# Kernel tuning notes

Measured on AMD Instinct MI355X. Metric: run time of the kernel, lower is better.

The kernel has to match this reference:

```python
import jax, jax.numpy as jnp
import numpy as np
import math

B, N, H, OUT = 32, 2048, 256, 128
K = 6            # knn_graph k
ALPHA = 0.2      # GCN2Conv alpha (beta=1 since theta/layer are None)
NEG = 0.2        # leaky_relu negative slope in ASAP
EPS = 1e-5       # batchnorm eps
RATIOS = (0.15, 0.25, 0.5)


def _scatter_add(vals, idx, n):
    # vals [B,E] or [B,E,h], idx [B,E] -> [B,n,...]
    b, e = idx.shape
    gi = (idx + jnp.arange(b)[:, None] * n).reshape(-1)
    flat = vals.reshape((b * e,) + vals.shape[2:])
    return jax.ops.segment_sum(flat, gi, num_segments=b * n).reshape((b, n) + vals.shape[2:])


def _scatter_max(vals, idx, n):
    b, e = idx.shape
    gi = (idx + jnp.arange(b)[:, None] * n).reshape(-1)
    flat = vals.reshape((b * e,) + vals.shape[2:])
    return jax.ops.segment_max(flat, gi, num_segments=b * n).reshape((b, n) + vals.shape[2:])


def _gather(x, idx):
    # x [B,n,...] or [B,n], idx [B,E]
    if x.ndim == 3:
        return jnp.take_along_axis(x, idx[..., None], axis=1)
    return jnp.take_along_axis(x, idx, axis=1)


def _knn_undirected(pos):
    # knn_graph(pos, k=6, loop=True) then to_undirected (coalesced via `valid` mask)
    b, n, _ = pos.shape
    d2 = jnp.sum((pos[:, :, None, :] - pos[:, None, :, :]) ** 2, axis=-1)  # [B,n,n]
    _, nbr = jax.lax.top_k(-d2, K)                # self included (dist 0)
    ctr = jnp.broadcast_to(jnp.arange(n)[None, :, None], (b, n, K)).reshape(b, n * K)
    nbr = nbr.reshape(b, n * K)
    src = jnp.concatenate([nbr, ctr], axis=1)     # symmetrize
    dst = jnp.concatenate([ctr, nbr], axis=1)
    key = src * n + dst
    order = jnp.argsort(key, axis=1)
    src = jnp.take_along_axis(src, order, axis=1)
    dst = jnp.take_along_axis(dst, order, axis=1)
    key = jnp.take_along_axis(key, order, axis=1)
    valid = jnp.concatenate([jnp.ones((b, 1), bool), key[:, 1:] != key[:, :-1]], axis=1)
    return src, dst, valid


def _edge_mlp(pos, src, dst, valid, W1, b1, g, be, m, v, W2, b2):
    # relu(MLP([1,32,1])(||p_i - p_j||)); BN in eval mode; self loops replaced by 1
    d = jnp.linalg.norm(_gather(pos, src) - _gather(pos, dst), axis=-1)  # [B,E]
    t = d[..., None] @ W1 + b1                       # [B,E,32]
    t = (t - m) * jax.lax.rsqrt(v + EPS) * g + be
    t = jax.nn.relu(t)
    w = jax.nn.relu((t @ W2 + b2)[..., 0])
    w = jnp.where(src == dst, 1.0, w)                # add_remaining_self_loops fill=1
    return jnp.where(valid, w, 0.0)                  # coalesce duplicate edges


def _gcn2(x, x0, src, dst, w, Wc):
    # GCN2Conv with beta=1, shared weights: ((1-a)*A_hat x + a*x0) @ W
    n = x.shape[1]
    deg = _scatter_add(w, dst, n)
    dis = jax.lax.rsqrt(jnp.maximum(deg, 1e-12))     # deg >= 1 (self loops)
    norm = _gather(dis, src) * w * _gather(dis, dst)
    agg = _scatter_add(norm[..., None] * _gather(x, src), dst, n)
    return ((1.0 - ALPHA) * agg + ALPHA * x0) @ Wc


def _asap(x, src, dst, valid, w, kpool, Wrel, brel, Wroot, Wlin, blin, Watt, batt,
          lW1, lb1, lW2, lW3, lb3):
    n = x.shape[1]
    # gnn_intra_cluster: GraphConv (add aggregation)
    x_pool = _scatter_add(w[..., None] * _gather(x, src), dst, n) @ Wrel + brel + x @ Wroot
    mj = _gather(x_pool, src)                                    # [B,E,H]
    x_q = _scatter_max(jnp.where(valid[..., None], mj, -jnp.inf), dst, n) @ Wlin + blin
    score = (jnp.concatenate([_gather(x_q, dst), mj], axis=-1) @ Watt + batt)[..., 0]
    score = jnp.where(valid, jax.nn.leaky_relu(score, NEG), -jnp.inf)
    smax = _scatter_max(score, dst, n)
    e = jnp.where(valid, jnp.exp(score - _gather(smax, dst)), 0.0)
    att = e / _gather(_scatter_add(e, dst, n), dst)
    xn = _scatter_add(att[..., None] * _gather(x, src), dst, n)
    # LEConv fitness (no edge weights; duplicates masked)
    a = (xn @ lW1 + lb1)[..., 0]
    bb = (xn @ lW2)[..., 0]
    msg = jnp.where(valid, _gather(a, src) - _gather(bb, dst), 0.0)
    fit = jax.nn.sigmoid(_scatter_add(msg, dst, n) + (xn @ lW3 + lb3)[..., 0])
    vals, idx = jax.lax.top_k(fit, kpool)
    return _gather(xn, idx) * vals[..., None], idx


def _forward(x, pos, conv_W, eW1, eb1, ebn_g, ebn_b, ebn_m, ebn_v, eW2, eb2,
             aWrel, abrel, aWroot, aWlin, ablin, aWatt, abatt,
             leW1, leb1, leW2, leW3, leb3, gW, gb, nW, nb):
    h = None
    readouts = []
    for s in range(4):
        src, dst, valid = _knn_undirected(pos)
        w = _edge_mlp(pos, src, dst, valid, eW1[s], eb1[s], ebn_g[s], ebn_b[s],
                      ebn_m[s], ebn_v[s], eW2[s], eb2[s])
        if s in (1, 2):
            readouts.append(jnp.concatenate([jnp.mean(h, axis=1), jnp.max(h, axis=1)], axis=-1))
        hin = x if s == 0 else h
        h = jax.nn.relu(_gcn2(hin, x, src, dst, w, conv_W[s]))
        if s < 3:
            kpool = math.ceil(RATIOS[s] * h.shape[1])
            h, idx = _asap(h, src, dst, valid, w, kpool, aWrel[s], abrel[s], aWroot[s],
                           aWlin[s], ablin[s], aWatt[s], abatt[s],
                           leW1[s], leb1[s], leW2[s], leW3[s], leb3[s])
            x = _gather(x, idx)
            pos = _gather(pos, idx)
    gate = jax.nn.softmax(h @ gW + gb, axis=1)      # attentional aggregation
    gp = jnp.sum(gate * (h @ nW + nb), axis=1)      # [B,OUT]
    return jnp.concatenate([gp, readouts[1], readouts[0]], axis=-1)


def setup_inputs() -> dict:
    key = jax.random.key(0)
    ks = iter(jax.random.split(key, 40))
    def rn(shape, scale=1.0):
        return scale * jax.random.normal(next(ks), shape, dtype=jnp.float32)
    return {
        "x": rn((B, N, H)),
        "pos": rn((B, N, 3)),
        "conv_W": rn((4, H, H), H ** -0.5),
        "eW1": rn((4, 1, 32)),
        "eb1": rn((4, 32), 0.1),
        "ebn_g": 1.0 + rn((4, 32), 0.1),
        "ebn_b": rn((4, 32), 0.1),
        "ebn_m": rn((4, 32), 0.1),
        "ebn_v": jnp.ones((4, 32), jnp.float32),
        "eW2": rn((4, 32, 1), 32 ** -0.5),
        "eb2": rn((4, 1), 0.1),
        "aWrel": rn((3, H, H), H ** -0.5),
        "abrel": rn((3, H), 0.1),
        "aWroot": rn((3, H, H), H ** -0.5),
        "aWlin": rn((3, H, H), H ** -0.5),
        "ablin": rn((3, H), 0.1),
        "aWatt": rn((3, 2 * H, 1), (2 * H) ** -0.5),
        "abatt": rn((3, 1), 0.1),
        "leW1": rn((3, H, 1), H ** -0.5),
        "leb1": rn((3, 1), 0.1),
        "leW2": rn((3, H, 1), H ** -0.5),
        "leW3": rn((3, H, 1), H ** -0.5),
        "leb3": rn((3, 1), 0.1),
        "gW": rn((H, 1), H ** -0.5),
        "gb": rn((1,), 0.1),
        "nW": rn((H, OUT), H ** -0.5),
        "nb": rn((OUT,), 0.1),
    }


def reference(x, pos, conv_W, eW1, eb1, ebn_g, ebn_b, ebn_m, ebn_v, eW2, eb2,
              aWrel, abrel, aWroot, aWlin, ablin, aWatt, abatt,
              leW1, leb1, leW2, leW3, leb3, gW, gb, nW, nb):
    return _forward(x, pos, conv_W, eW1, eb1, ebn_g, ebn_b, ebn_m, ebn_v, eW2, eb2,
                    aWrel, abrel, aWroot, aWlin, ablin, aWatt, abatt,
                    leW1, leb1, leW2, leW3, leb3, gW, gb, nW, nb)
```

## Files before the change

kernel.cpp:

```cpp
#include <hip/hip_runtime.h>
#include <hip/hip_bf16.h>
#include <math.h>

#define BB 32
#define NMAX 2048
#define HD 256
#define KNN 6
#define OUTD 128
#define NCH 8

typedef __hip_bfloat16 bf16;

__global__ void k_detect(const void* __restrict__ x, int* __restrict__ flag){
  __shared__ int cnt_s;
  if (threadIdx.x==0) cnt_s=0;
  __syncthreads();
  const unsigned short* u=(const unsigned short*)x;
  int c=0;
  for (int i=threadIdx.x;i<4096;i+=256){
    int e=(u[i]>>7)&0xFF;
    if (e>=0xC0) c++;
  }
  atomicAdd(&cnt_s,c);
  __syncthreads();
  if (threadIdx.x==0) flag[0]=(cnt_s>32)?1:0;
}

__device__ __forceinline__ float loadx(const void* x, int fl, size_t idx){
  if (fl) return ((const float*)x)[idx];
  unsigned short u=((const unsigned short*)x)[idx];
  return __uint_as_float(((unsigned)u)<<16);
}
__device__ __forceinline__ float4 loadx4(const void* x, int fl, size_t idx){
  if (fl) return *(const float4*)((const float*)x+idx);
  float4 r;
  r.x=loadx(x,0,idx); r.y=loadx(x,0,idx+1); r.z=loadx(x,0,idx+2); r.w=loadx(x,0,idx+3);
  return r;
}

__global__ void k_cvtpos(const void* __restrict__ pos, const int* __restrict__ flag,
                         float* __restrict__ posF){
  int t=blockIdx.x*256+threadIdx.x;
  if (t>=BB*NMAX*3) return;
  posF[t]=loadx(pos,flag[0],t);
}
struct WTab { const void* src[25]; int cnt[25]; int dst[25]; };
__global__ void k_cvtw(WTab tab, const int* __restrict__ flag, float* __restrict__ wsW){
  int seg=blockIdx.y;
  int t=blockIdx.x*256+threadIdx.x;
  if (t>=tab.cnt[seg]) return;
  wsW[tab.dst[seg]+t]=loadx(tab.src[seg],flag[0],t);
}

__global__ void k_initcum(int* __restrict__ cum){
  int t=blockIdx.x*256+threadIdx.x;
  if (t<BB*NMAX) cum[t]=t%NMAX;
}
__global__ void k_zero2(int* __restrict__ a, int* __restrict__ b, int n){
  int t=blockIdx.x*256+threadIdx.x;
  if (t<n){ a[t]=0; b[t]=0; }
}
__global__ void k_gatherpos(const float* __restrict__ posF, const int* __restrict__ cum,
                            float* __restrict__ posf, int n){
  int t=blockIdx.x*256+threadIdx.x;
  if (t>=BB*n*3) return;
  int c=t%3, i=(t/3)%n, b=t/(3*n);
  posf[t]=posF[((size_t)b*NMAX+cum[b*NMAX+i])*3+c];
}

__global__ void k_knn_part(const float* __restrict__ posf, double* __restrict__ dcand,
                           int* __restrict__ icand, int n){
  int b=blockIdx.z, ch=blockIdx.y;
  int i=blockIdx.x*256+threadIdx.x;
  const float* pp=posf+(size_t)b*n*3;
  int cs=(n+NCH-1)/NCH;
  int jlo=ch*cs, jhi=jlo+cs; if (jhi>n) jhi=n;
  double px=0.0,py=0.0,pz=0.0;
  if (i<n){ px=(double)pp[i*3]; py=(double)pp[i*3+1]; pz=(double)pp[i*3+2]; }
  double bd0=INFINITY,bd1=INFINITY,bd2=INFINITY,bd3=INFINITY,bd4=INFINITY,bd5=INFINITY;
  int   bi0=0x7fffffff,bi1=0x7fffffff,bi2=0x7fffffff,bi3=0x7fffffff,bi4=0x7fffffff,bi5=0x7fffffff;
  __shared__ double sx[256],sy[256],sz[256];
  for (int base=jlo;base<jhi;base+=256){
    int j=base+threadIdx.x;
    if (j<jhi){ sx[threadIdx.x]=(double)pp[j*3]; sy[threadIdx.x]=(double)pp[j*3+1]; sz[threadIdx.x]=(double)pp[j*3+2]; }
    __syncthreads();
    int lim=jhi-base; if (lim>256) lim=256;
    if (i<n){
      for (int t=0;t<lim;t++){
        double dx=__dsub_rn(px,sx[t]);
        double dy=__dsub_rn(py,sy[t]);
        double dz=__dsub_rn(pz,sz[t]);
        double d2=__dadd_rn(__dadd_rn(__dmul_rn(dx,dx),__dmul_rn(dy,dy)),__dmul_rn(dz,dz));
        if (d2<bd5){
          int id=base+t;
          if (d2<bd4){ bd5=bd4; bi5=bi4;
            if (d2<bd3){ bd4=bd3; bi4=bi3;
              if (d2<bd2){ bd3=bd2; bi3=bi2;
                if (d2<bd1){ bd2=bd1; bi2=bi1;
                  if (d2<bd0){ bd1=bd0; bi1=bi0; bd0=d2; bi0=id; }
                  else { bd1=d2; bi1=id; }
                } else { bd2=d2; bi2=id; }
              } else { bd3=d2; bi3=id; }
            } else { bd4=d2; bi4=id; }
          } else { bd5=d2; bi5=id; }
        }
      }
    }
    __syncthreads();
  }
  if (i<n){
    size_t o=(((size_t)b*NCH+ch)*n+i)*KNN;
    dcand[o+0]=bd0; dcand[o+1]=bd1; dcand[o+2]=bd2; dcand[o+3]=bd3; dcand[o+4]=bd4; dcand[o+5]=bd5;
    icand[o+0]=bi0; icand[o+1]=bi1; icand[o+2]=bi2; icand[o+3]=bi3; icand[o+4]=bi4; icand[o+5]=bi5;
  }
}

__global__ void k_knn_merge(const double* __restrict__ dcand, const int* __restrict__ icand,
                            int* __restrict__ nbr, int n){
  int t=blockIdx.x*256+threadIdx.x;
  if (t>=BB*n) return;
  int b=t/n, i=t-b*n;
  double cd[NCH*KNN]; int ci[NCH*KNN];
  #pragma unroll
  for (int ch=0;ch<NCH;ch++){
    size_t o=(((size_t)b*NCH+ch)*n+i)*KNN;
    #pragma unroll
    for (int k=0;k<KNN;k++){ cd[ch*KNN+k]=dcand[o+k]; ci[ch*KNN+k]=icand[o+k]; }
  }
  int* out=nbr+(size_t)t*KNN;
  #pragma unroll
  for (int k=0;k<KNN;k++){
    int best=0;
    for (int q=1;q<NCH*KNN;q++){
      bool lt=(cd[q]<cd[best])||(cd[q]==cd[best]&&ci[q]<ci[best]);
      if (lt) best=q;
    }
    out[k]=ci[best];
    cd[best]=INFINITY; ci[best]=0x7fffffff;
  }
}

__global__ void k_edge(const float* __restrict__ posf, const int* __restrict__ nbr,
                       float* __restrict__ w1, float* __restrict__ w2,
                       unsigned char* __restrict__ val2, int* __restrict__ cnt,
                       const float* __restrict__ W1, const float* __restrict__ b1,
                       const float* __restrict__ g,  const float* __restrict__ be,
                       const float* __restrict__ m,  const float* __restrict__ v,
                       const float* __restrict__ W2, const float* __restrict__ b2p,
                       int n){
  int t=blockIdx.x*256+threadIdx.x;
  if (t>=BB*n*KNN) return;
  int k=t%KNN; int c=(t/KNN)%n; int b=t/(KNN*n);
  const int* nb=nbr+(size_t)b*n*KNN;
  int j=nb[c*KNN+k];
  atomicAdd(&cnt[b*n+j],1);
  bool dup=false;
  #pragma unroll
  for (int kk=0;kk<KNN;kk++) dup=dup||(nb[j*KNN+kk]==c);
  const float* pp=posf+(size_t)b*n*3;
  double dx=__dsub_rn((double)pp[c*3+0],(double)pp[j*3+0]);
  double dy=__dsub_rn((double)pp[c*3+1],(double)pp[j*3+1]);
  double dz=__dsub_rn((double)pp[c*3+2],(double)pp[j*3+2]);
  double d2=__dadd_rn(__dadd_rn(__dmul_rn(dx,dx),__dmul_rn(dy,dy)),__dmul_rn(dz,dz));
  float dd=(float)sqrt(d2);
  float wv;
  if (j==c) wv=1.0f;
  else {
    float acc=b2p[0];
    for (int q=0;q<32;q++){
      float tt=dd*W1[q]+b1[q];
      float r=1.0f/sqrtf(v[q]+1e-5f);
      tt=(tt-m[q])*r*g[q]+be[q];
      tt=fmaxf(tt,0.f);
      acc=fmaf(tt,W2[q],acc);
    }
    wv=fmaxf(acc,0.f);
  }
  w1[t]=wv;
  w2[t]=dup?0.f:wv;
  val2[t]=dup?0:1;
}

__global__ void k_csr_scan(const int* __restrict__ cnt, int* __restrict__ offs, int n){
  int b=blockIdx.x, t=threadIdx.x;
  int L=(n+255)/256;
  __shared__ int ssum[256];
  int lo=t*L, hi=lo+L; if (hi>n) hi=n; if (lo>n) lo=n;
  int s=0;
  for (int i=lo;i<hi;i++) s+=cnt[b*n+i];
  ssum[t]=s;
  __syncthreads();
  if (t==0){
    int run=0;
    for (int q=0;q<256;q++){ int vv=ssum[q]; ssum[q]=run; run+=vv; }
  }
  __syncthreads();
  int run=ssum[t];
  for (int i=lo;i<hi;i++){ offs[b*(n+1)+i]=run; run+=cnt[b*n+i]; }
  if (lo<n && hi==n) offs[b*(n+1)+n]=run;
}
__global__ void k_csr_fill(const int* __restrict__ nbr, const int* __restrict__ offs,
                           int* __restrict__ cur, int* __restrict__ rev, int n){
  int t=blockIdx.x*256+threadIdx.x;
  if (t>=BB*n*KNN) return;
  int b=t/(n*KNN); int rem=t-b*n*KNN;
  int d=nbr[t];
  int slot=offs[b*(n+1)+d]+atomicAdd(&cur[b*n+d],1);
  if (slot<0) slot=0;
  if (slot>=n*KNN) slot=n*KNN-1;
  rev[(size_t)b*n*KNN+slot]=rem;
}
__global__ void k_csr_sort(int* __restrict__ rev, const int* __restrict__ offs, int n){
  int t=blockIdx.x*256+threadIdx.x;
  if (t>=BB*n) return;
  int b=t/n, d=t-b*n;
  size_t base=(size_t)b*n*KNN;
  int lo=offs[b*(n+1)+d], hi=offs[b*(n+1)+d+1];
  for (int a2=lo+1;a2<hi;a2++){
    int vv=rev[base+a2]; int p=a2;
    while (p>lo && rev[base+p-1]>vv){ rev[base+p]=rev[base+p-1]; p--; }
    rev[base+p]=vv;
  }
}

__global__ void k_degdis(const float* __restrict__ w1, const float* __restrict__ w2,
                         const int* __restrict__ rev, const int* __restrict__ offs,
                         float* __restrict__ dis, int n){
  int t=blockIdx.x*256+threadIdx.x;
  if (t>=BB*n) return;
  int b=t/n, d=t-b*n;
  size_t rbase=(size_t)b*n*KNN;
  float s=0.f;
  #pragma unroll
  for (int k=0;k<KNN;k++) s+=w1[(size_t)t*KNN+k];
  int lo=offs[b*(n+1)+d], hi=offs[b*(n+1)+d+1];
  for (int sl=lo;sl<hi;sl++) s+=w2[rbase+rev[rbase+sl]];
  dis[t]=1.0f/sqrtf(fmaxf(s,1e-12f));
}

template<int MODE,int RAW>
__global__ void k_nbrsum(const float* __restrict__ Hin, const float* __restrict__ w1,
                         const float* __restrict__ w2, const int* __restrict__ nbr,
                         const int* __restrict__ rev, const int* __restrict__ offs,
                         const float* __restrict__ dis, const void* __restrict__ xraw,
                         const int* __restrict__ flag,
                         const int* __restrict__ cum, float* __restrict__ outp, int n){
  int wid=blockIdx.x*4+(threadIdx.x>>6);
  int lane=threadIdx.x&63;
  if (wid>=BB*n) return;
  int b=wid/n, d=wid-b*n;
  int fl=flag[0];
  const float* Hb=Hin+(size_t)b*n*HD;
  float4 a=make_float4(0.f,0.f,0.f,0.f);
  float dd=(MODE==0)?dis[wid]:0.f;
  int c4=lane*4;
  #pragma unroll
  for (int k=0;k<KNN;k++){
    int sN=nbr[(size_t)wid*KNN+k];
    float wv=w1[(size_t)wid*KNN+k];
    float nm=(MODE==0)?dis[b*n+sN]*wv*dd:wv;
    float4 r = RAW ? loadx4(xraw,fl,((size_t)b*n+sN)*HD+c4)
                   : *(const float4*)(Hb+(size_t)sN*HD+c4);
    a.x=fmaf(nm,r.x,a.x); a.y=fmaf(nm,r.y,a.y); a.z=fmaf(nm,r.z,a.z); a.w=fmaf(nm,r.w,a.w);
  }
  size_t rbase=(size_t)b*n*KNN;
  int lo=offs[b*(n+1)+d], hi=offs[b*(n+1)+d+1];
  for (int sl=lo;sl<hi;sl++){
    int e=rev[rbase+sl];
    int sN=e/KNN;
    float wv=w2[rbase+e];
    float nm=(MODE==0)?dis[b*n+sN]*wv*dd:wv;
    float4 r = RAW ? loadx4(xraw,fl,((size_t)b*n+sN)*HD+c4)
                   : *(const float4*)(Hb+(size_t)sN*HD+c4);
    a.x=fmaf(nm,r.x,a.x); a.y=fmaf(nm,r.y,a.y); a.z=fmaf(nm,r.z,a.z); a.w=fmaf(nm,r.w,a.w);
  }
  if (MODE==0){
    float4 xr=loadx4(xraw,fl,((size_t)b*NMAX+cum[b*NMAX+d])*HD+c4);
    a.x=0.8f*a.x+0.2f*xr.x; a.y=0.8f*a.y+0.2f*xr.y;
    a.z=0.8f*a.z+0.2f*xr.z; a.w=0.8f*a.w+0.2f*xr.w;
  }
  *(float4*)(outp+(size_t)wid*HD+c4)=a;
}

__global__ void k_mm(const float* __restrict__ A1, const float* __restrict__ B1,
                     const float* __restrict__ A2, const float* __restrict__ B2,
                     const float* __restrict__ bias, int relu,
                     float* __restrict__ Cout, int M){
  __shared__ __align__(16) float As[16][68];
  __shared__ __align__(16) float Bs[16][260];
  int tid=threadIdx.x, bm=blockIdx.x;
  int tm=tid>>4, tn=tid&15;
  float acc[4][4][4];
  #pragma unroll
  for (int b2=0;b2<4;b2++){
    #pragma unroll
    for (int i=0;i<4;i++){
      #pragma unroll
      for (int j=0;j<4;j++) acc[b2][i][j]=0.f;
    }
  }
  int l=tid*4;
  int ar=l>>4, ak=l&15;
  int arow=bm*64+ar;
  int KT = A2 ? 512 : 256;
  for (int k0=0;k0<KT;k0+=16){
    const float* Asrc=(k0<HD)?A1:A2;
    const float* Bsrc=(k0<HD)?B1:B2;
    int kc=k0&(HD-1);
    if (arow<M){
      float4 a4=*(const float4*)(Asrc+(size_t)arow*HD+kc+ak);
      As[ak][ar]=a4.x; As[ak+1][ar]=a4.y; As[ak+2][ar]=a4.z; As[ak+3][ar]=a4.w;
    } else {
      As[ak][ar]=0.f; As[ak+1][ar]=0.f; As[ak+2][ar]=0.f; As[ak+3][ar]=0.f;
    }
    #pragma unroll
    for (int c=0;c<4;c++){
      int idx=c*256+tid;
      int rkk=idx>>6, cc=(idx&63)*4;
      *(float4*)&Bs[rkk][cc]=*(const float4*)(Bsrc+(size_t)(kc+rkk)*HD+cc);
    }
    __syncthreads();
    #pragma unroll
    for (int kk=0;kk<16;kk++){
      float4 av=*(const float4*)&As[kk][tm*4];
      #pragma unroll
      for (int b2=0;b2<4;b2++){
        float4 bv=*(const float4*)&Bs[kk][b2*64+tn*4];
        acc[b2][0][0]=fmaf(av.x,bv.x,acc[b2][0][0]); acc[b2][0][1]=fmaf(av.x,bv.y,acc[b2][0][1]);
        acc[b2][0][2]=fmaf(av.x,bv.z,acc[b2][0][2]); acc[b2][0][3]=fmaf(av.x,bv.w,acc[b2][0][3]);
        acc[b2][1][0]=fmaf(av.y,bv.x,acc[b2][1][0]); acc[b2][1][1]=fmaf(av.y,bv.y,acc[b2][1][1]);
        acc[b2][1][2]=fmaf(av.y,bv.z,acc[b2][1][2]); acc[b2][1][3]=fmaf(av.y,bv.w,acc[b2][1][3]);
        acc[b2][2][0]=fmaf(av.z,bv.x,acc[b2][2][0]); acc[b2][2][1]=fmaf(av.z,bv.y,acc[b2][2][1]);
        acc[b2][2][2]=fmaf(av.z,bv.z,acc[b2][2][2]); acc[b2][2][3]=fmaf(av.z,bv.w,acc[b2][2][3]);
        acc[b2][3][0]=fmaf(av.w,bv.x,acc[b2][3][0]); acc[b2][3][1]=fmaf(av.w,bv.y,acc[b2][3][1]);
        acc[b2][3][2]=fmaf(av.w,bv.z,acc[b2][3][2]); acc[b2][3][3]=fmaf(av.w,bv.w,acc[b2][3][3]);
      }
    }
    __syncthreads();
  }
  #pragma unroll
  for (int i=0;i<4;i++){
    int grow=bm*64+tm*4+i;
    if (grow>=M) continue;
    #pragma unroll
    for (int b2=0;b2<4;b2++){
      #pragma unroll
      for (int j=0;j<4;j++){
        int gcol=b2*64+tn*4+j;
        float v=acc[b2][i][j];
        if (bias) v+=bias[gcol];
        if (relu) v=fmaxf(v,0.f);
        Cout[(size_t)grow*HD+gcol]=v;
      }
    }
  }
}

__global__ void k_va(const float* __restrict__ Wlin, const float* __restrict__ wa,
                     const float* __restrict__ blin, float* __restrict__ va){
  int i=threadIdx.x;
  float acc=0.f;
  for (int j=0;j<HD;j++) acc=fmaf(Wlin[(size_t)i*HD+j],wa[j],acc);
  va[i]=acc;
  if (i==0){
    float c=0.f;
    for (int j=0;j<HD;j++) c=fmaf(blin[j],wa[j],c);
    va[256]=c;
  }
}

__global__ void k_qd(const float* __restrict__ T, const float* __restrict__ wb,
                     const float* __restrict__ va, const int* __restrict__ nbr,
                     const int* __restrict__ rev, const int* __restrict__ offs,
                     const unsigned char* __restrict__ val2,
                     float* __restrict__ pb, float* __restrict__ qd, int n){
  int wid=blockIdx.x*4+(threadIdx.x>>6);
  int lane=threadIdx.x&63;
  if (wid>=BB*n) return;
  int b=wid/n, d=wid-b*n;
  int c4=lane*4;
  float4 r1=*(const float4*)(T+(size_t)wid*HD+c4);
  float4 wb4=*(const float4*)(wb+c4);
  float p=r1.x*wb4.x+r1.y*wb4.y+r1.z*wb4.z+r1.w*wb4.w;
  const float* Tb=T+(size_t)b*n*HD;
  float4 m4=make_float4(-INFINITY,-INFINITY,-INFINITY,-INFINITY);
  #pragma unroll
  for (int k=0;k<KNN;k++){
    int sN=nbr[(size_t)wid*KNN+k];
    float4 r=*(const float4*)(Tb+(size_t)sN*HD+c4);
    m4.x=fmaxf(m4.x,r.x); m4.y=fmaxf(m4.y,r.y); m4.z=fmaxf(m4.z,r.z); m4.w=fmaxf(m4.w,r.w);
  }
  size_t rbase=(size_t)b*n*KNN;
  int lo=offs[b*(n+1)+d], hi=offs[b*(n+1)+d+1];
  for (int sl=lo;sl<hi;sl++){
    int e=rev[rbase+sl];
    if (!val2[rbase+e]) continue;
    int sN=e/KNN;
    float4 r=*(const float4*)(Tb+(size_t)sN*HD+c4);
    m4.x=fmaxf(m4.x,r.x); m4.y=fmaxf(m4.y,r.y); m4.z=fmaxf(m4.z,r.z); m4.w=fmaxf(m4.w,r.w);
  }
  float4 va4=*(const float4*)(va+c4);
  float q=va4.x*m4.x+va4.y*m4.y+va4.z*m4.z+va4.w*m4.w;
  #pragma unroll
  for (int o=32;o>0;o>>=1){ p+=__shfl_xor(p,o); q+=__shfl_xor(q,o); }
  if (lane==0){ pb[wid]=p; qd[wid]=q+va[256]; }
}

__global__ void k_attxn(const float* __restrict__ Hin, const float* __restrict__ pb,
                        const float* __restrict__ qd, const int* __restrict__ nbr,
                        const int* __restrict__ rev, const int* __restrict__ offs,
                        const unsigned char* __restrict__ val2, const float* __restrict__ abatt,
                        float* __restrict__ Tout, int n){
  int wid=blockIdx.x*4+(threadIdx.x>>6);
  int lane=threadIdx.x&63;
  if (wid>=BB*n) return;
  int b=wid/n, d=wid-b*n;
  float batt=abatt[0];
  float qs=qd[wid];
  const float* Hb=Hin+(size_t)b*n*HD;
  int c4=lane*4;
  size_t rbase=(size_t)b*n*KNN;
  int lo=offs[b*(n+1)+d], hi=offs[b*(n+1)+d+1];
  float smax=-INFINITY;
  #pragma unroll
  for (int k=0;k<KNN;k++){
    int sN=nbr[(size_t)wid*KNN+k];
    float sc=qs+pb[b*n+sN]+batt;
    sc=sc>=0.f?sc:0.2f*sc;
    smax=fmaxf(smax,sc);
  }
  for (int sl=lo;sl<hi;sl++){
    int e=rev[rbase+sl];
    if (!val2[rbase+e]) continue;
    int sN=e/KNN;
    float sc=qs+pb[b*n+sN]+batt;
    sc=sc>=0.f?sc:0.2f*sc;
    smax=fmaxf(smax,sc);
  }
  float es=0.f;
  float4 a=make_float4(0.f,0.f,0.f,0.f);
  #pragma unroll
  for (int k=0;k<KNN;k++){
    int sN=nbr[(size_t)wid*KNN+k];
    float sc=qs+pb[b*n+sN]+batt;
    sc=sc>=0.f?sc:0.2f*sc;
    float e2=expf(sc-smax);
    es+=e2;
    float4 r=*(const float4*)(Hb+(size_t)sN*HD+c4);
    a.x=fmaf(e2,r.x,a.x); a.y=fmaf(e2,r.y,a.y); a.z=fmaf(e2,r.z,a.z); a.w=fmaf(e2,r.w,a.w);
  }
  for (int sl=lo;sl<hi;sl++){
    int e=rev[rbase+sl];
    if (!val2[rbase+e]) continue;
    int sN=e/KNN;
    float sc=qs+pb[b*n+sN]+batt;
    sc=sc>=0.f?sc:0.2f*sc;
    float e2=expf(sc-smax);
    es+=e2;
    float4 r=*(const float4*)(Hb+(size_t)sN*HD+c4);
    a.x=fmaf(e2,r.x,a.x); a.y=fmaf(e2,r.y,a.y); a.z=fmaf(e2,r.z,a.z); a.w=fmaf(e2,r.w,a.w);
  }
  float inv=1.f/es;
  a.x*=inv; a.y*=inv; a.z*=inv; a.w*=inv;
  *(float4*)(Tout+(size_t)wid*HD+c4)=a;
}

__global__ void k_ledots(const float* __restrict__ T, const float* __restrict__ lW1,
                         const float* __restrict__ lb1, const float* __restrict__ lW2,
                         const float* __restrict__ lW3, const float* __restrict__ lb3,
                         float* __restrict__ av, float* __restrict__ bbv,
                         float* __restrict__ l3v, int n){
  int wid=blockIdx.x*4+(threadIdx.x>>6);
  int lane=threadIdx.x&63;
  if (wid>=BB*n) return;
  int c4=lane*4;
  float4 r=*(const float4*)(T+(size_t)wid*HD+c4);
  float4 w1v=*(const float4*)(lW1+c4);
  float4 w2v=*(const float4*)(lW2+c4);
  float4 w3v=*(const float4*)(lW3+c4);
  float s1=r.x*w1v.x+r.y*w1v.y+r.z*w1v.z+r.w*w1v.w;
  float s2=r.x*w2v.x+r.y*w2v.y+r.z*w2v.z+r.w*w2v.w;
  float s3=r.x*w3v.x+r.y*w3v.y+r.z*w3v.z+r.w*w3v.w;
  #pragma unroll
  for (int o=32;o>0;o>>=1){ s1+=__shfl_xor(s1,o); s2+=__shfl_xor(s2,o); s3+=__shfl_xor(s3,o); }
  if (lane==0){ av[wid]=s1+lb1[0]; bbv[wid]=s2; l3v[wid]=s3+lb3[0]; }
}

__global__ void k_fit(const float* __restrict__ av, const float* __restrict__ bbv,
                      const float* __restrict__ l3v, const int* __restrict__ nbr,
                      const int* __restrict__ rev, const int* __restrict__ offs,
                      const unsigned char* __restrict__ val2, float* __restrict__ fit, int n){
  int t=blockIdx.x*256+threadIdx.x;
  if (t>=BB*n) return;
  int b=t/n, d=t-b*n;
  size_t rbase=(size_t)b*n*KNN;
  float ms=0.f; int cv=KNN;
  #pragma unroll
  for (int k=0;k<KNN;k++) ms+=av[b*n+nbr[(size_t)t*KNN+k]];
  int lo=offs[b*(n+1)+d], hi=offs[b*(n+1)+d+1];
  for (int sl=lo;sl<hi;sl++){
    int e=rev[rbase+sl];
    if (val2[rbase+e]){ ms+=av[b*n+e/KNN]; cv++; }
  }
  float z=ms-(float)cv*bbv[t]+l3v[t];
  fit[t]=1.f/(1.f+expf(-z));
}

__global__ void k_rank(const float* __restrict__ fit, float* __restrict__ svl,
                       int* __restrict__ sid, int n, int kp){
  int t=blockIdx.x*256+threadIdx.x;
  if (t>=BB*n) return;
  int b=t/n, i=t-b*n;
  float fi=fit[t];
  const float* fb=fit+(size_t)b*n;
  int rank=0;
  for (int j=0;j<n;j++){
    float fj=fb[j];
    if (fj>fi || (fj==fi && j<i)) rank++;
  }
  if (rank<kp){ svl[b*NMAX+rank]=fi; sid[b*NMAX+rank]=i; }
}

__global__ void k_pool(const float* __restrict__ T, const float* __restrict__ svl,
                       const int* __restrict__ sid, const int* __restrict__ cumA,
                       int* __restrict__ cumB, float* __restrict__ Hout, int n, int kp){
  int wid=blockIdx.x*4+(threadIdx.x>>6);
  int lane=threadIdx.x&63;
  if (wid>=BB*kp) return;
  int b=wid/kp, j=wid-b*kp;
  int srcn=sid[b*NMAX+j];
  if (srcn<0) srcn=0;
  if (srcn>=n) srcn=n-1;
  float vv=svl[b*NMAX+j];
  int c4=lane*4;
  float4 r=*(const float4*)(T+((size_t)b*n+srcn)*HD+c4);
  r.x*=vv; r.y*=vv; r.z*=vv; r.w*=vv;
  *(float4*)(Hout+((size_t)b*kp+j)*HD+c4)=r;
  if (lane==0) cumB[b*NMAX+j]=cumA[b*NMAX+srcn];
}

__global__ void k_readout(const float* __restrict__ Hb, float* __restrict__ ro, int n){
  int b=blockIdx.x, h=threadIdx.x;
  const float* p=Hb+(size_t)b*n*HD+h;
  float s=0.f, m=-INFINITY;
  for (int i=0;i<n;i++){ float v=p[(size_t)i*HD]; s+=v; m=fmaxf(m,v); }
  ro[b*512+h]=s/(float)n;
  ro[b*512+256+h]=m;
}

__global__ void k_final(const float* __restrict__ Hb, const float* __restrict__ gW,
                        const float* __restrict__ gb, const float* __restrict__ nW,
                        const float* __restrict__ nbias, const float* __restrict__ ro0,
                        const float* __restrict__ ro1, float* __restrict__ outp, int n){
  int b=blockIdx.x, tid=threadIdx.x;
  int wv=tid>>6, lane=tid&63;
  __shared__ float gate[64];
  for (int i=wv;i<n;i+=4){
    const float* r=Hb+((size_t)b*n+i)*HD;
    float p=0.f;
    for (int h=lane;h<HD;h+=64) p=fmaf(r[h],gW[h],p);
    #pragma unroll
    for (int o=32;o>0;o>>=1) p+=__shfl_xor(p,o);
    if (lane==0) gate[i]=p+gb[0];
  }
  __syncthreads();
  if (tid==0){
    float mx=-INFINITY;
    for (int i=0;i<n;i++) mx=fmaxf(mx,gate[i]);
    float sm=0.f;
    for (int i=0;i<n;i++){ gate[i]=expf(gate[i]-mx); sm+=gate[i]; }
    float inv=1.f/sm;
    for (int i=0;i<n;i++) gate[i]*=inv;
  }
  __syncthreads();
  if (tid<OUTD){
    float acc=0.f;
    for (int i=0;i<n;i++){
      const float* r=Hb+((size_t)b*n+i)*HD;
      float dot=0.f;
      for (int h=0;h<HD;h++) dot=fmaf(r[h],nW[(size_t)h*OUTD+tid],dot);
      acc=fmaf(gate[i],dot+nbias[tid],acc);
    }
    outp[(size_t)b*1152+tid]=acc;
  }
  for (int q=tid;q<512;q+=256){
    outp[(size_t)b*1152+128+q]=ro1[b*512+q];
    outp[(size_t)b*1152+640+q]=ro0[b*512+q];
  }
}

extern "C" void kernel_launch(void* const* d_in, const int* in_sizes, int n_in,
                              void* d_out, int out_size, void* d_ws, size_t ws_size,
                              hipStream_t stream){
  if (n_in<27) return;
  if (in_sizes[0]!=BB*NMAX*HD || in_sizes[1]!=BB*NMAX*3) return;
  float* outp=(float*)d_out;
  (void)out_size;

  char* p=(char*)d_ws;
  auto carve=[&](size_t bytes)->char*{ char* r=p; p+=((bytes+255)/256)*256; return r; };
  float* posF=(float*)carve((size_t)BB*NMAX*3*4);
  float* posf=(float*)carve((size_t)BB*NMAX*3*4);
  float* Hbuf=(float*)carve((size_t)BB*NMAX*HD*4);
  float* Tbuf=(float*)carve((size_t)BB*NMAX*HD*4);
  static const int wcnt[25]={262144,128,128,128,128,128,128,128,4,
                             196608,768,196608,196608,768,1536,3,
                             768,3,768,768,3,256,1,32768,128};
  int woff[25]; int wtot=0;
  for (int i=0;i<25;i++){ woff[i]=wtot; wtot+=(wcnt[i]+63)&~63; }
  float* wsW=(float*)carve((size_t)wtot*4);
  int*   nbr =(int*)  carve((size_t)BB*NMAX*KNN*4);
  int*   rev =(int*)  carve((size_t)BB*NMAX*KNN*4);
  float* w1  =(float*)carve((size_t)BB*NMAX*KNN*4);
  float* w2  =(float*)carve((size_t)BB*NMAX*KNN*4);
  unsigned char* val2=(unsigned char*)carve((size_t)BB*NMAX*KNN);
  int* cnt  =(int*)carve((size_t)BB*NMAX*4);
  int* offs =(int*)carve((size_t)BB*(NMAX+1)*4);
  int* cur  =(int*)carve((size_t)BB*NMAX*4);
  float* dis=(float*)carve((size_t)BB*NMAX*4);
  float* pb =(float*)carve((size_t)BB*NMAX*4);
  float* qd =(float*)carve((size_t)BB*NMAX*4);
  float* av =(float*)carve((size_t)BB*NMAX*4);
  float* bbv=(float*)carve((size_t)BB*NMAX*4);
  float* l3v=(float*)carve((size_t)BB*NMAX*4);
  float* fit=(float*)carve((size_t)BB*NMAX*4);
  float* svl=(float*)carve((size_t)BB*NMAX*4);
  int*   sid=(int*)  carve((size_t)BB*NMAX*4);
  int* cumA =(int*)carve((size_t)BB*NMAX*4);
  int* cumB =(int*)carve((size_t)BB*NMAX*4);
  int* flag =(int*)carve(256);
  float* va =(float*)carve(272*4);
  float* ro0=(float*)carve((size_t)BB*512*4);
  float* ro1=(float*)carve((size_t)BB*512*4);
  size_t need=(size_t)(p-(char*)d_ws);
  if (ws_size<need) return;

  double* dcand=(double*)Tbuf;
  int*    icand=(int*)((char*)Tbuf + (size_t)BB*NCH*NMAX*KNN*8);

  k_detect<<<1,256,0,stream>>>(d_in[0],flag);
  k_cvtpos<<<(BB*NMAX*3+255)/256,256,0,stream>>>(d_in[1],flag,posF);
  {
    WTab tab;
    int maxc=0;
    for (int i=0;i<25;i++){ tab.src[i]=d_in[2+i]; tab.cnt[i]=wcnt[i]; tab.dst[i]=woff[i]; if (wcnt[i]>maxc) maxc=wcnt[i]; }
    k_cvtw<<<dim3((maxc+255)/256,25),256,0,stream>>>(tab,flag,wsW);
  }
  k_initcum<<<(BB*NMAX+255)/256,256,0,stream>>>(cumA);

  const int NS[4]={2048,308,77,39};
  const int KP[3]={308,77,39};

  for (int s=0;s<4;s++){
    int n=NS[s]; int M=BB*n;
    const float* wconv =wsW+woff[0]+(size_t)s*65536;
    const float* eW1p  =wsW+woff[1]+s*32;
    const float* eb1p  =wsW+woff[2]+s*32;
    const float* gp    =wsW+woff[3]+s*32;
    const float* bep   =wsW+woff[4]+s*32;
    const float* mp    =wsW+woff[5]+s*32;
    const float* vp    =wsW+woff[6]+s*32;
    const float* W2p   =wsW+woff[7]+s*32;
    const float* b2p   =wsW+woff[8]+s;
    const float* aWrelp=wsW+woff[9]+(size_t)s*65536;
    const float* abrelp=wsW+woff[10]+s*256;
    const float* aWrootp=wsW+woff[11]+(size_t)s*65536;
    const float* aWlinp=wsW+woff[12]+(size_t)s*65536;
    const float* ablinp=wsW+woff[13]+s*256;
    const float* wap   =wsW+woff[14]+s*512;
    const float* wbp   =wsW+woff[14]+s*512+256;
    const float* abattp=wsW+woff[15]+s;
    const float* leW1p =wsW+woff[16]+s*256;
    const float* leb1p =wsW+woff[17]+s;
    const float* leW2p =wsW+woff[18]+s*256;
    const float* leW3p =wsW+woff[19]+s*256;
    const float* leb3p =wsW+woff[20]+s;

    k_gatherpos<<<(BB*n*3+255)/256,256,0,stream>>>(posF,cumA,posf,n);
    k_knn_part<<<dim3((n+255)/256,NCH,BB),256,0,stream>>>(posf,dcand,icand,n);
    k_knn_merge<<<(BB*n+255)/256,256,0,stream>>>(dcand,icand,nbr,n);
    int totE=BB*n*KNN;
    k_zero2<<<(BB*n+255)/256,256,0,stream>>>(cnt,cur,BB*n);
    k_edge<<<(totE+255)/256,256,0,stream>>>(posf,nbr,w1,w2,val2,cnt,
        eW1p,eb1p,gp,bep,mp,vp,W2p,b2p,n);
    k_csr_scan<<<BB,256,0,stream>>>(cnt,offs,n);
    k_csr_fill<<<(totE+255)/256,256,0,stream>>>(nbr,offs,cur,rev,n);
    k_csr_sort<<<(BB*n+255)/256,256,0,stream>>>(rev,offs,n);
    if (s==1) k_readout<<<BB,256,0,stream>>>(Hbuf,ro0,n);
    if (s==2) k_readout<<<BB,256,0,stream>>>(Hbuf,ro1,n);
    k_degdis<<<(BB*n+255)/256,256,0,stream>>>(w1,w2,rev,offs,dis,n);
    if (s==0)
      k_nbrsum<0,1><<<(BB*n+3)/4,256,0,stream>>>(nullptr,w1,w2,nbr,rev,offs,dis,d_in[0],flag,cumA,Tbuf,n);
    else
      k_nbrsum<0,0><<<(BB*n+3)/4,256,0,stream>>>(Hbuf,w1,w2,nbr,rev,offs,dis,d_in[0],flag,cumA,Tbuf,n);
    k_mm<<<(M+63)/64,256,0,stream>>>(Tbuf,wconv,(const float*)nullptr,(const float*)nullptr,
                                     (const float*)nullptr,1,Hbuf,M);
    if (s<3){
      int kp=KP[s];
      k_nbrsum<1,0><<<(BB*n+3)/4,256,0,stream>>>(Hbuf,w1,w2,nbr,rev,offs,dis,d_in[0],flag,cumA,Tbuf,n);
      k_mm<<<(M+63)/64,256,0,stream>>>(Tbuf,aWrelp,Hbuf,aWrootp,abrelp,0,Tbuf,M);
      k_va<<<1,256,0,stream>>>(aWlinp,wap,ablinp,va);
      k_qd<<<(BB*n+3)/4,256,0,stream>>>(Tbuf,wbp,va,nbr,rev,offs,val2,pb,qd,n);
      k_attxn<<<(BB*n+3)/4,256,0,stream>>>(Hbuf,pb,qd,nbr,rev,offs,val2,abattp,Tbuf,n);
      k_ledots<<<(BB*n+3)/4,256,0,stream>>>(Tbuf,leW1p,leb1p,leW2p,leW3p,leb3p,av,bbv,l3v,n);
      k_fit<<<(BB*n+255)/256,256,0,stream>>>(av,bbv,l3v,nbr,rev,offs,val2,fit,n);
      k_rank<<<(BB*n+255)/256,256,0,stream>>>(fit,svl,sid,n,kp);
      k_pool<<<(BB*kp+3)/4,256,0,stream>>>(Tbuf,svl,sid,cumA,cumB,Hbuf,n,kp);
      { int* t=cumA; cumA=cumB; cumB=t; }
    }
  }
  k_final<<<BB,256,0,stream>>>(Hbuf,wsW+woff[21],wsW+woff[22],wsW+woff[23],wsW+woff[24],
                               ro0,ro1,outp,NS[3]);
}
```

Before: 2.351 ms.

## Retile matmul to 8x8 per thread, fuse ledots into attxn, stage rank in LDS

The fp32 GEMM switches from four 4x4 sub-tiles per thread to one contiguous 8x8 tile per thread, which changes the LDS read pattern and register reuse. The leader-score dot products move into the attention aggregation kernel, so one launch and a full reread of T are removed. The rank kernel copies each batch's fitness vector into shared memory and launches with a 2D grid, so the O(n^2) comparisons read LDS instead of global memory. The 8-column-per-thread B reads may hit LDS bank conflicts, and the output stores are less coalesced.

```diff
diff --git a/kernel.cpp b/kernel.cpp
--- a/kernel.cpp
+++ b/kernel.cpp
@@ -289,15 +289,12 @@
   __shared__ __align__(16) float As[16][68];
   __shared__ __align__(16) float Bs[16][260];
   int tid=threadIdx.x, bm=blockIdx.x;
-  int tm=tid>>4, tn=tid&15;
-  float acc[4][4][4];
-  #pragma unroll
-  for (int b2=0;b2<4;b2++){
+  int tr=tid>>5, tc=tid&31;
+  float acc[8][8];
+  #pragma unroll
+  for (int i=0;i<8;i++){
     #pragma unroll
-    for (int i=0;i<4;i++){
-      #pragma unroll
-      for (int j=0;j<4;j++) acc[b2][i][j]=0.f;
-    }
+    for (int j=0;j<8;j++) acc[i][j]=0.f;
   }
   int l=tid*4;
   int ar=l>>4, ak=l&15;
@@ -322,36 +319,30 @@
     __syncthreads();
     #pragma unroll
     for (int kk=0;kk<16;kk++){
-      float4 av=*(const float4*)&As[kk][tm*4];
+      float af[8], bf[8];
+      *(float4*)&af[0]=*(const float4*)&As[kk][tr*8];
+      *(float4*)&af[4]=*(const float4*)&As[kk][tr*8+4];
+      *(float4*)&bf[0]=*(const float4*)&Bs[kk][tc*8];
+      *(float4*)&bf[4]=*(const float4*)&Bs[kk][tc*8+4];
       #pragma unroll
-      for (int b2=0;b2<4;b2++){
-        float4 bv=*(const float4*)&Bs[kk][b2*64+tn*4];
-        acc[b2][0][0]=fmaf(av.x,bv.x,acc[b2][0][0]); acc[b2][0][1]=fmaf(av.x,bv.y,acc[b2][0][1]);
-        acc[b2][0][2]=fmaf(av.x,bv.z,acc[b2][0][2]); acc[b2][0][3]=fmaf(av.x,bv.w,acc[b2][0][3]);
-        acc[b2][1][0]=fmaf(av.y,bv.x,acc[b2][1][0]); acc[b2][1][1]=fmaf(av.y,bv.y,acc[b2][1][1]);
-        acc[b2][1][2]=fmaf(av.y,bv.z,acc[b2][1][2]); acc[b2][1][3]=fmaf(av.y,bv.w,acc[b2][1][3]);
-        acc[b2][2][0]=fmaf(av.z,bv.x,acc[b2][2][0]); acc[b2][2][1]=fmaf(av.z,bv.y,acc[b2][2][1]);
-        acc[b2][2][2]=fmaf(av.z,bv.z,acc[b2][2][2]); acc[b2][2][3]=fmaf(av.z,bv.w,acc[b2][2][3]);
-        acc[b2][3][0]=fmaf(av.w,bv.x,acc[b2][3][0]); acc[b2][3][1]=fmaf(av.w,bv.y,acc[b2][3][1]);
-        acc[b2][3][2]=fmaf(av.w,bv.z,acc[b2][3][2]); acc[b2][3][3]=fmaf(av.w,bv.w,acc[b2][3][3]);
+      for (int i=0;i<8;i++){
+        #pragma unroll
+        for (int j=0;j<8;j++) acc[i][j]=fmaf(af[i],bf[j],acc[i][j]);
       }
     }
     __syncthreads();
   }
   #pragma unroll
-  for (int i=0;i<4;i++){
-    int grow=bm*64+tm*4+i;
+  for (int i=0;i<8;i++){
+    int grow=bm*64+tr*8+i;
     if (grow>=M) continue;
     #pragma unroll
-    for (int b2=0;b2<4;b2++){
-      #pragma unroll
-      for (int j=0;j<4;j++){
-        int gcol=b2*64+tn*4+j;
-        float v=acc[b2][i][j];
-        if (bias) v+=bias[gcol];
-        if (relu) v=fmaxf(v,0.f);
-        Cout[(size_t)grow*HD+gcol]=v;
-      }
+    for (int j=0;j<8;j++){
+      int gcol=tc*8+j;
+      float v=acc[i][j];
+      if (bias) v+=bias[gcol];
+      if (relu) v=fmaxf(v,0.f);
+      Cout[(size_t)grow*HD+gcol]=v;
     }
   }
 }
@@ -410,6 +401,10 @@
                         const float* __restrict__ qd, const int* __restrict__ nbr,
                         const int* __restrict__ rev, const int* __restrict__ offs,
                         const unsigned char* __restrict__ val2, const float* __restrict__ abatt,
+                        const float* __restrict__ lW1, const float* __restrict__ lb1,
+                        const float* __restrict__ lW2, const float* __restrict__ lW3,
+                        const float* __restrict__ lb3,
+                        float* __restrict__ av, float* __restrict__ bbv, float* __restrict__ l3v,
                         float* __restrict__ Tout, int n){
   int wid=blockIdx.x*4+(threadIdx.x>>6);
   int lane=threadIdx.x&63;
@@ -463,24 +458,12 @@
   float inv=1.f/es;
   a.x*=inv; a.y*=inv; a.z*=inv; a.w*=inv;
   *(float4*)(Tout+(size_t)wid*HD+c4)=a;
-}
-
-__global__ void k_ledots(const float* __restrict__ T, const float* __restrict__ lW1,
-                         const float* __restrict__ lb1, const float* __restrict__ lW2,
-                         const float* __restrict__ lW3, const float* __restrict__ lb3,
-                         float* __restrict__ av, float* __restrict__ bbv,
-                         float* __restrict__ l3v, int n){
-  int wid=blockIdx.x*4+(threadIdx.x>>6);
-  int lane=threadIdx.x&63;
-  if (wid>=BB*n) return;
-  int c4=lane*4;
-  float4 r=*(const float4*)(T+(size_t)wid*HD+c4);
   float4 w1v=*(const float4*)(lW1+c4);
   float4 w2v=*(const float4*)(lW2+c4);
   float4 w3v=*(const float4*)(lW3+c4);
-  float s1=r.x*w1v.x+r.y*w1v.y+r.z*w1v.z+r.w*w1v.w;
-  float s2=r.x*w2v.x+r.y*w2v.y+r.z*w2v.z+r.w*w2v.w;
-  float s3=r.x*w3v.x+r.y*w3v.y+r.z*w3v.z+r.w*w3v.w;
+  float s1=a.x*w1v.x+a.y*w1v.y+a.z*w1v.z+a.w*w1v.w;
+  float s2=a.x*w2v.x+a.y*w2v.y+a.z*w2v.z+a.w*w2v.w;
+  float s3=a.x*w3v.x+a.y*w3v.y+a.z*w3v.z+a.w*w3v.w;
   #pragma unroll
   for (int o=32;o>0;o>>=1){ s1+=__shfl_xor(s1,o); s2+=__shfl_xor(s2,o); s3+=__shfl_xor(s3,o); }
   if (lane==0){ av[wid]=s1+lb1[0]; bbv[wid]=s2; l3v[wid]=s3+lb3[0]; }
@@ -508,14 +491,17 @@
 
 __global__ void k_rank(const float* __restrict__ fit, float* __restrict__ svl,
                        int* __restrict__ sid, int n, int kp){
-  int t=blockIdx.x*256+threadIdx.x;
-  if (t>=BB*n) return;
-  int b=t/n, i=t-b*n;
-  float fi=fit[t];
+  __shared__ float sf[2048];
+  int b=blockIdx.y;
+  int i=blockIdx.x*256+threadIdx.x;
   const float* fb=fit+(size_t)b*n;
+  for (int j=threadIdx.x;j<n;j+=256) sf[j]=fb[j];
+  __syncthreads();
+  if (i>=n) return;
+  float fi=sf[i];
   int rank=0;
   for (int j=0;j<n;j++){
-    float fj=fb[j];
+    float fj=sf[j];
     if (fj>fi || (fj==fi && j<i)) rank++;
   }
   if (rank<kp){ svl[b*NMAX+rank]=fi; sid[b*NMAX+rank]=i; }
@@ -701,10 +687,10 @@
       k_mm<<<(M+63)/64,256,0,stream>>>(Tbuf,aWrelp,Hbuf,aWrootp,abrelp,0,Tbuf,M);
       k_va<<<1,256,0,stream>>>(aWlinp,wap,ablinp,va);
       k_qd<<<(BB*n+3)/4,256,0,stream>>>(Tbuf,wbp,va,nbr,rev,offs,val2,pb,qd,n);
-      k_attxn<<<(BB*n+3)/4,256,0,stream>>>(Hbuf,pb,qd,nbr,rev,offs,val2,abattp,Tbuf,n);
-      k_ledots<<<(BB*n+3)/4,256,0,stream>>>(Tbuf,leW1p,leb1p,leW2p,leW3p,leb3p,av,bbv,l3v,n);
+      k_attxn<<<(BB*n+3)/4,256,0,stream>>>(Hbuf,pb,qd,nbr,rev,offs,val2,abattp,
+                                           leW1p,leb1p,leW2p,leW3p,leb3p,av,bbv,l3v,Tbuf,n);
       k_fit<<<(BB*n+255)/256,256,0,stream>>>(av,bbv,l3v,nbr,rev,offs,val2,fit,n);
-      k_rank<<<(BB*n+255)/256,256,0,stream>>>(fit,svl,sid,n,kp);
+      k_rank<<<dim3((n+255)/256,BB),256,0,stream>>>(fit,svl,sid,n,kp);
       k_pool<<<(BB*kp+3)/4,256,0,stream>>>(Tbuf,svl,sid,cumA,cumB,Hbuf,n,kp);
       { int* t=cumA; cumA=cumB; cumB=t; }
     }
```

Measured after the change: 2.212 ms. 1.06x faster.
